# Kernel optimization log

Hardware: AMD Instinct MI355X
Metric: run time of the kernel (lower is better)

## Reference

```python
import jax, jax.numpy as jnp
import numpy as np

S, B, D, H, DH = 512, 32, 256, 8, 32  # seq, batch, in_dim, heads, dim_head
LN_EPS = 1e-5


def setup_inputs() -> dict:
    key = jax.random.key(0)
    k1, k2, k3 = jax.random.split(key, 3)
    x = jax.random.normal(k1, (S, B, D), jnp.float32)
    slow_W = jax.random.normal(k2, (H * (5 * DH + 2), D), jnp.float32) * 0.02
    out_W = jax.random.normal(k3, (D, H * DH), jnp.float32) * 0.02
    ln_g = jnp.ones((D,), jnp.float32)
    ln_b = jnp.zeros((D,), jnp.float32)
    return {"x": x, "slow_W": slow_W, "out_W": out_W, "ln_g": ln_g, "ln_b": ln_b}


def elu_p1(x):
    return jax.nn.elu(x) + 1.0


def sum_norm(x):
    return x / jnp.sum(x, axis=-1, keepdims=True)


def layer_norm(x, g, b):
    mu = jnp.mean(x, axis=-1, keepdims=True)
    var = jnp.mean(jnp.square(x - mu), axis=-1, keepdims=True)
    return (x - mu) * jax.lax.rsqrt(var + LN_EPS) * g + b


def _fast_rnn_forward(x, slow_W, out_W, ln_g, ln_b):
    slen, bsz, _ = x.shape
    o = layer_norm(x, ln_g, ln_b)
    qkv = jnp.einsum('sbd,ed->sbe', o, slow_W)  # [S,B,H*(5*DH+2)]
    qkv = qkv.reshape(slen, bsz, H, 5 * DH + 2)
    q, k, v, rk, rv, beta, rbeta = jnp.split(
        qkv, [DH, 2 * DH, 3 * DH, 4 * DH, 5 * DH, 5 * DH + 1], axis=-1)
    beta = jax.nn.sigmoid(beta)      # [S,B,H,1]
    rbeta = jax.nn.sigmoid(rbeta)    # [S,B,H,1]
    q = sum_norm(elu_p1(q))
    k = sum_norm(elu_p1(k))
    rk = jax.nn.softmax(rk, axis=-1)

    # ---- feed-forward fast weights with delta rule (fast_weight_delta) ----
    def ff_step(W, inp):
        qt, kt, vt, bt = inp                      # [B,H,DH], bt [B,H,1]
        v_old = jnp.einsum('bhij,bhj->bhi', W, kt)
        W = W + ((bt * (vt - v_old))[..., :, None] * kt[..., None, :])
        z = jnp.einsum('bhij,bhj->bhi', W, qt)
        return W, z

    W0 = jnp.zeros((bsz, H, DH, DH), x.dtype)
    _, z = jax.lax.scan(ff_step, W0, (q, k, v, beta))  # z: [S,B,H,DH]

    # ---- recurrent fast weights (fast_rnn_v2): query = softmax(prev state) ----
    def rec_step(carry, inp):
        R, h = carry
        zt, kt, vt, bt = inp
        q_rec = jax.nn.softmax(h, axis=-1)         # query from previous state
        v_old = jnp.einsum('bhij,bhj->bhi', R, kt)
        R = R + ((bt * (vt - v_old))[..., :, None] * kt[..., None, :])
        h = zt + jnp.einsum('bhij,bhj->bhi', R, q_rec)
        return (R, h), h

    R0 = jnp.zeros((bsz, H, DH, DH), x.dtype)
    h0 = jnp.zeros((bsz, H, DH), x.dtype)
    _, hs = jax.lax.scan(rec_step, (R0, h0), (z, rk, rv, rbeta))  # [S,B,H,DH]

    out = hs.reshape(slen, bsz, H * DH)
    out = jnp.einsum('sbe,de->sbd', out, out_W)
    return x + out  # dropout is identity in eval


def reference(x, slow_W, out_W, ln_g, ln_b):
    return _fast_rnn_forward(x, slow_W, out_W, ln_g, ln_b)
```

## Files before the change

### kernel.cpp

```cpp
#include <hip/hip_runtime.h>
#include <hip/hip_bf16.h>
#include <math.h>

#define S_   512
#define B_   32
#define D_   256
#define H_   8
#define DH_  32
#define E_   (H_*(5*DH_+2))
#define SB_  (S_*B_)
#define LN_EPSF 1e-5f

#define ROWP_ 164
#define CH2_  32
#define NC2_  (S_/CH2_)
#define NPAD_ 1344

typedef short  bf16x8 __attribute__((ext_vector_type(8)));
typedef float  f32x4  __attribute__((ext_vector_type(4)));

__device__ __forceinline__ float wave_sum64(float v){
  #pragma unroll
  for (int m = 32; m >= 1; m >>= 1) v += __shfl_xor(v, m, 64);
  return v;
}
__device__ __forceinline__ float gsum32(float v){
  #pragma unroll
  for (int m = 16; m >= 1; m >>= 1) v += __shfl_xor(v, m, 32);
  return v;
}
__device__ __forceinline__ float gmax32(float v){
  #pragma unroll
  for (int m = 16; m >= 1; m >>= 1) v = fmaxf(v, __shfl_xor(v, m, 32));
  return v;
}

#if __has_builtin(__builtin_amdgcn_permlane32_swap)
typedef int v2i_ __attribute__((ext_vector_type(2)));
__device__ __forceinline__ float xhalf_sum(float x){
  v2i_ r = __builtin_amdgcn_permlane32_swap(__float_as_int(x), __float_as_int(x), false, false);
  return __int_as_float(r.x) + __int_as_float(r.y);
}
#else
__device__ __forceinline__ float xhalf_sum(float x){
  return x + __shfl_xor(x, 32, 64);
}
#endif

__device__ __forceinline__ void gl16(const float* g, float* l){
  __builtin_amdgcn_global_load_lds(
      (const __attribute__((address_space(1))) unsigned int*)g,
      (__attribute__((address_space(3))) unsigned int*)l, 16, 0, 0);
}
__device__ __forceinline__ void stage_plane32(const float* gb, int fieldOff,
                                              float* plane, int lane){
  const int tt = lane >> 3, dd = (lane & 7) << 2;
  #pragma unroll
  for (int i = 0; i < 4; i++)
    gl16(gb + (size_t)(8*i + tt)*ROWP_ + fieldOff + dd, plane + i*256);
}
__device__ __forceinline__ void stage_beta32(const float* gb, float* bpl, int lane){
  if (lane < CH2_) gl16(gb + (size_t)lane*ROWP_ + 5*DH_, bpl);
}

__global__ __launch_bounds__(256) void ln_kernel(const float* __restrict__ x,
                                                 const float* __restrict__ g,
                                                 const float* __restrict__ b,
                                                 __hip_bfloat16* __restrict__ o){
  __shared__ float sbuf[4];
  const int row = blockIdx.x, tid = threadIdx.x;
  const float v = x[(size_t)row*D_ + tid];
  float s = wave_sum64(v);
  if ((tid & 63) == 0) sbuf[tid >> 6] = s;
  __syncthreads();
  const float mu = (sbuf[0]+sbuf[1]+sbuf[2]+sbuf[3]) * (1.f/D_);
  __syncthreads();
  const float d = v - mu;
  float s2 = wave_sum64(d*d);
  if ((tid & 63) == 0) sbuf[tid >> 6] = s2;
  __syncthreads();
  const float var = (sbuf[0]+sbuf[1]+sbuf[2]+sbuf[3]) * (1.f/D_);
  const float rstd = rsqrtf(var + LN_EPSF);
  o[(size_t)row*D_ + tid] = __float2bfloat16(d*rstd*g[tid] + b[tid]);
}

__global__ __launch_bounds__(256) void cvt_w1(const float* __restrict__ W,
                                              __hip_bfloat16* __restrict__ o){
  const int r = blockIdx.x, c = threadIdx.x;
  const float v = (r < E_) ? W[(size_t)r*D_ + c] : 0.f;
  o[(size_t)r*D_ + c] = __float2bfloat16(v);
}
__global__ __launch_bounds__(256) void cvt_w2(const float* __restrict__ W,
                                              __hip_bfloat16* __restrict__ o){
  const size_t i = (size_t)blockIdx.x*256 + threadIdx.x;
  o[i] = __float2bfloat16(W[i]);
}

__global__ __launch_bounds__(256) void gemm1_mfma(const __hip_bfloat16* __restrict__ A,
                                                  const __hip_bfloat16* __restrict__ Bw,
                                                  float* __restrict__ qkvT){
  const int tid = threadIdx.x;
  const int w = tid >> 6, l = tid & 63;
  const int lr = l & 15, lk = (l >> 4) << 3;
  const int m0 = blockIdx.y*64 + (w>>1)*32;
  const int n0 = blockIdx.x*64 + (w&1)*32;

  const __hip_bfloat16* Ap = A  + (size_t)(m0+lr)*D_ + lk;
  const __hip_bfloat16* Bp = Bw + (size_t)(n0+lr)*D_ + lk;

  f32x4 acc00={0,0,0,0}, acc01={0,0,0,0}, acc10={0,0,0,0}, acc11={0,0,0,0};
  #pragma unroll
  for (int ks = 0; ks < 8; ++ks){
    const bf16x8 a0 = *(const bf16x8*)(Ap + ks*32);
    const bf16x8 a1 = *(const bf16x8*)(Ap + 16*D_ + ks*32);
    const bf16x8 b0 = *(const bf16x8*)(Bp + ks*32);
    const bf16x8 b1 = *(const bf16x8*)(Bp + 16*D_ + ks*32);
    acc00 = __builtin_amdgcn_mfma_f32_16x16x32_bf16(a0, b0, acc00, 0,0,0);
    acc01 = __builtin_amdgcn_mfma_f32_16x16x32_bf16(a0, b1, acc01, 0,0,0);
    acc10 = __builtin_amdgcn_mfma_f32_16x16x32_bf16(a1, b0, acc10, 0,0,0);
    acc11 = __builtin_amdgcn_mfma_f32_16x16x32_bf16(a1, b1, acc11, 0,0,0);
  }

  const int mrow = (l>>4)<<2;
  #pragma unroll
  for (int i=0;i<2;i++){
    #pragma unroll
    for (int j=0;j<2;j++){
      const f32x4 av = (i==0) ? (j==0?acc00:acc01) : (j==0?acc10:acc11);
      const int n = n0 + j*16 + lr;
      if (n < E_){
        const unsigned head = (unsigned)n / 162u;
        const unsigned jj   = (unsigned)n - head*162u;
        #pragma unroll
        for (int reg=0;reg<4;reg++){
          const int m = m0 + i*16 + mrow + reg;
          const int s = m >> 5, bq = m & 31;
          qkvT[((size_t)(bq*8u+head)*S_ + s)*ROWP_ + jj] = av[reg];
        }
      }
    }
  }
}

__global__ __launch_bounds__(256) void gemm2_mfma(const __hip_bfloat16* __restrict__ A,
                                                  const __hip_bfloat16* __restrict__ Bw,
                                                  const float* __restrict__ X,
                                                  float* __restrict__ C){
  const int tid = threadIdx.x;
  const int w = tid >> 6, l = tid & 63;
  const int lr = l & 15, lk = (l >> 4) << 3;
  const int m0 = blockIdx.y*64 + (w>>1)*32;
  const int n0 = blockIdx.x*64 + (w&1)*32;

  const __hip_bfloat16* Ap = A  + (size_t)(m0+lr)*D_ + lk;
  const __hip_bfloat16* Bp = Bw + (size_t)(n0+lr)*D_ + lk;

  f32x4 acc00={0,0,0,0}, acc01={0,0,0,0}, acc10={0,0,0,0}, acc11={0,0,0,0};
  #pragma unroll
  for (int ks = 0; ks < 8; ++ks){
    const bf16x8 a0 = *(const bf16x8*)(Ap + ks*32);
    const bf16x8 a1 = *(const bf16x8*)(Ap + 16*D_ + ks*32);
    const bf16x8 b0 = *(const bf16x8*)(Bp + ks*32);
    const bf16x8 b1 = *(const bf16x8*)(Bp + 16*D_ + ks*32);
    acc00 = __builtin_amdgcn_mfma_f32_16x16x32_bf16(a0, b0, acc00, 0,0,0);
    acc01 = __builtin_amdgcn_mfma_f32_16x16x32_bf16(a0, b1, acc01, 0,0,0);
    acc10 = __builtin_amdgcn_mfma_f32_16x16x32_bf16(a1, b0, acc10, 0,0,0);
    acc11 = __builtin_amdgcn_mfma_f32_16x16x32_bf16(a1, b1, acc11, 0,0,0);
  }

  const int mrow = (l>>4)<<2;
  #pragma unroll
  for (int i=0;i<2;i++){
    #pragma unroll
    for (int j=0;j<2;j++){
      const f32x4 av = (i==0) ? (j==0?acc00:acc01) : (j==0?acc10:acc11);
      const int n = n0 + j*16 + lr;
      #pragma unroll
      for (int reg=0;reg<4;reg++){
        const size_t m = (size_t)(m0 + i*16 + mrow + reg);
        C[m*D_ + n] = av[reg] + X[m*D_ + n];
      }
    }
  }
}

__global__ __launch_bounds__(256) void act2_kernel(float* __restrict__ qkvT){
  const int row = blockIdx.x*8 + (threadIdx.x >> 5);
  const int i = threadIdx.x & 31;
  float* base = qkvT + (size_t)row*ROWP_;
  float qv  = base[i];
  float kv  = base[DH_ + i];
  float rkv = base[3*DH_ + i];
  qv = qv > 0.f ? qv + 1.f : __expf(qv);
  kv = kv > 0.f ? kv + 1.f : __expf(kv);
  const float qs = gsum32(qv);
  const float ks = gsum32(kv);
  const float rm = gmax32(rkv);
  const float re = __expf(rkv - rm);
  const float rs = gsum32(re);
  base[i]         = qv / qs;
  base[DH_ + i]   = kv / ks;
  base[3*DH_ + i] = re / rs;
  if (i < 2){
    const float bv = base[5*DH_ + i];
    base[5*DH_ + i] = 1.f/(1.f + __expf(-bv));
  }
}

__global__ __launch_bounds__(64,1) void scan_fused(const float* __restrict__ qkvT,
                                                   __hip_bfloat16* __restrict__ hsb){
  const int pair = blockIdx.x;
  const int lane = threadIdx.x;
  const int r = lane & 31, p = lane >> 5;
  const int b = pair >> 3, hh = pair & 7;
  const float* gbase = qkvT + (size_t)pair*S_*ROWP_;

  __shared__ __align__(16) float Lq [2][CH2_][DH_];
  __shared__ __align__(16) float Lk [2][CH2_][DH_];
  __shared__ __align__(16) float Lv [2][CH2_][DH_];
  __shared__ __align__(16) float Lrk[2][CH2_][DH_];
  __shared__ __align__(16) float Lrv[2][CH2_][DH_];
  __shared__ __align__(16) float Lb [2][CH2_][4];
  __shared__ __align__(16) float ebuf[2][DH_];

  float W[16], R[16];
  #pragma unroll
  for (int i=0;i<16;i++){ W[i]=0.f; R[i]=0.f; }
  float h = 0.f;

  stage_plane32(gbase, 0,      &Lq [0][0][0], lane);
  stage_plane32(gbase, DH_,    &Lk [0][0][0], lane);
  stage_plane32(gbase, 2*DH_,  &Lv [0][0][0], lane);
  stage_plane32(gbase, 3*DH_,  &Lrk[0][0][0], lane);
  stage_plane32(gbase, 4*DH_,  &Lrv[0][0][0], lane);
  stage_beta32 (gbase,         &Lb [0][0][0], lane);
  asm volatile("s_waitcnt vmcnt(0)" ::: "memory");

  for (int c = 0; c < NC2_; ++c){
    const int bi = c & 1;
    if (c+1 < NC2_){
      const float* gnext = gbase + (size_t)(c+1)*CH2_*ROWP_;
      stage_plane32(gnext, 0,      &Lq [bi^1][0][0], lane);
      stage_plane32(gnext, DH_,    &Lk [bi^1][0][0], lane);
      stage_plane32(gnext, 2*DH_,  &Lv [bi^1][0][0], lane);
      stage_plane32(gnext, 3*DH_,  &Lrk[bi^1][0][0], lane);
      stage_plane32(gnext, 4*DH_,  &Lrv[bi^1][0][0], lane);
      stage_beta32 (gnext,         &Lb [bi^1][0][0], lane);
    }
    const int s0 = c*CH2_;
    #pragma unroll 2
    for (int t = 0; t < CH2_; ++t){
      const float e = __expf(h);
      if (!p) ebuf[t&1][r] = e;

      float q[16], k[16], rk[16];
      #pragma unroll
      for (int j=0;j<4;j++){
        *(float4*)&q[4*j]  = *(const float4*)&Lq [bi][t][p*16 + 4*j];
        *(float4*)&k[4*j]  = *(const float4*)&Lk [bi][t][p*16 + 4*j];
        *(float4*)&rk[4*j] = *(const float4*)&Lrk[bi][t][p*16 + 4*j];
      }
      const float vv  = Lv [bi][t][r];
      const float rvv = Lrv[bi][t][r];
      const float2 bet = *(const float2*)&Lb[bi][t][0];

      float a0=0.f,a1=0.f,a2=0.f,a3=0.f;
      #pragma unroll
      for (int c4=0;c4<16;c4+=4){
        a0=fmaf(W[c4+0],k[c4+0],a0); a1=fmaf(W[c4+1],k[c4+1],a1);
        a2=fmaf(W[c4+2],k[c4+2],a2); a3=fmaf(W[c4+3],k[c4+3],a3);
      }
      const float dot1f = xhalf_sum((a0+a1)+(a2+a3));
      const float coeff = bet.x*(vv - dot1f);
      float b0=0.f,b1=0.f,b2=0.f,b3=0.f;
      #pragma unroll
      for (int c4=0;c4<16;c4+=4){
        W[c4+0]=fmaf(coeff,k[c4+0],W[c4+0]); b0=fmaf(W[c4+0],q[c4+0],b0);
        W[c4+1]=fmaf(coeff,k[c4+1],W[c4+1]); b1=fmaf(W[c4+1],q[c4+1],b1);
        W[c4+2]=fmaf(coeff,k[c4+2],W[c4+2]); b2=fmaf(W[c4+2],q[c4+2],b2);
        W[c4+3]=fmaf(coeff,k[c4+3],W[c4+3]); b3=fmaf(W[c4+3],q[c4+3],b3);
      }
      const float z = xhalf_sum((b0+b1)+(b2+b3));

      float c0=0.f,c1=0.f,c2=0.f,c3=0.f;
      #pragma unroll
      for (int c4=0;c4<16;c4+=4){
        c0=fmaf(R[c4+0],rk[c4+0],c0); c1=fmaf(R[c4+1],rk[c4+1],c1);
        c2=fmaf(R[c4+2],rk[c4+2],c2); c3=fmaf(R[c4+3],rk[c4+3],c3);
      }
      const float dot1r = xhalf_sum((c0+c1)+(c2+c3));
      const float coefr = bet.y*(rvv - dot1r);
      #pragma unroll
      for (int c4=0;c4<16;c4+=4){
        R[c4+0]=fmaf(coefr,rk[c4+0],R[c4+0]); R[c4+1]=fmaf(coefr,rk[c4+1],R[c4+1]);
        R[c4+2]=fmaf(coefr,rk[c4+2],R[c4+2]); R[c4+3]=fmaf(coefr,rk[c4+3],R[c4+3]);
      }

      float ev[16];
      #pragma unroll
      for (int j=0;j<4;j++)
        *(float4*)&ev[4*j] = *(const float4*)&ebuf[t&1][p*16 + 4*j];

      float t0=(ev[0]+ev[1])+(ev[2]+ev[3]),   t1=(ev[4]+ev[5])+(ev[6]+ev[7]);
      float t2=(ev[8]+ev[9])+(ev[10]+ev[11]), t3=(ev[12]+ev[13])+(ev[14]+ev[15]);
      const float Ss = xhalf_sum((t0+t1)+(t2+t3));

      float d0=0.f,d1=0.f,d2=0.f,d3=0.f;
      #pragma unroll
      for (int c4=0;c4<16;c4+=4){
        d0=fmaf(R[c4+0],ev[c4+0],d0); d1=fmaf(R[c4+1],ev[c4+1],d1);
        d2=fmaf(R[c4+2],ev[c4+2],d2); d3=fmaf(R[c4+3],ev[c4+3],d3);
      }
      const float dot2 = xhalf_sum((d0+d1)+(d2+d3));

      h = fmaf(dot2, __builtin_amdgcn_rcpf(Ss), z);
      if (!p) hsb[((size_t)(s0+t)*B_ + b)*D_ + hh*DH_ + r] = __float2bfloat16(h);
    }
    asm volatile("s_waitcnt vmcnt(0)" ::: "memory");
  }
}

extern "C" void kernel_launch(void* const* d_in, const int* in_sizes, int n_in,
                              void* d_out, int out_size, void* d_ws, size_t ws_size,
                              hipStream_t stream) {
  const float* x      = (const float*)d_in[0];
  const float* slow_W = (const float*)d_in[1];
  const float* out_W  = (const float*)d_in[2];
  const float* ln_g   = (const float*)d_in[3];
  const float* ln_b   = (const float*)d_in[4];
  float* out = (float*)d_out;

  float* qkvT = (float*)d_ws;
  __hip_bfloat16* obf  = (__hip_bfloat16*)(qkvT + (size_t)B_*H_*S_*ROWP_);
  __hip_bfloat16* hsb  = obf;
  __hip_bfloat16* w1bf = obf + (size_t)SB_*D_;
  __hip_bfloat16* w2bf = w1bf + (size_t)NPAD_*D_;

  cvt_w1<<<NPAD_, 256, 0, stream>>>(slow_W, w1bf);
  cvt_w2<<<D_, 256, 0, stream>>>(out_W, w2bf);
  ln_kernel<<<SB_, 256, 0, stream>>>(x, ln_g, ln_b, obf);

  dim3 g1(NPAD_/64, SB_/64);
  gemm1_mfma<<<g1, 256, 0, stream>>>(obf, w1bf, qkvT);

  act2_kernel<<<B_*H_*S_/8, 256, 0, stream>>>(qkvT);

  scan_fused<<<B_*H_, 64, 0, stream>>>(qkvT, hsb);

  dim3 g2(D_/64, SB_/64);
  gemm2_mfma<<<g2, 256, 0, stream>>>(hsb, w2bf, x, out);
}
```

Before: 419.2 us.

## Prefetch scan inputs directly into registers with two-step software pipeline

Replaces the chunked LDS double-buffering in the recurrent scan kernel with direct global-to-register loads via inline asm. Two register sets hold the next two timesteps, and vmcnt waits are set by hand. This removes the LDS staging traffic and the per-chunk full waits. The cost is higher register pressure, a fragile hand-counted vmcnt scheme, and exposed global latency if two steps of lookahead are not enough. The hsb store is now done by all lanes, and the ebuf write is no longer guarded by p.

Measured after the change: 374.5 us. -10.7%, faster.

```diff
diff --git a/kernel.cpp b/kernel.cpp
--- a/kernel.cpp
+++ b/kernel.cpp
@@ -12,12 +12,11 @@
 #define LN_EPSF 1e-5f
 
 #define ROWP_ 164
-#define CH2_  32
-#define NC2_  (S_/CH2_)
 #define NPAD_ 1344
 
 typedef short  bf16x8 __attribute__((ext_vector_type(8)));
 typedef float  f32x4  __attribute__((ext_vector_type(4)));
+typedef float  f32x2  __attribute__((ext_vector_type(2)));
 
 __device__ __forceinline__ float wave_sum64(float v){
   #pragma unroll
@@ -47,21 +46,15 @@
 }
 #endif
 
-__device__ __forceinline__ void gl16(const float* g, float* l){
-  __builtin_amdgcn_global_load_lds(
-      (const __attribute__((address_space(1))) unsigned int*)g,
-      (__attribute__((address_space(3))) unsigned int*)l, 16, 0, 0);
-}
-__device__ __forceinline__ void stage_plane32(const float* gb, int fieldOff,
-                                              float* plane, int lane){
-  const int tt = lane >> 3, dd = (lane & 7) << 2;
-  #pragma unroll
-  for (int i = 0; i < 4; i++)
-    gl16(gb + (size_t)(8*i + tt)*ROWP_ + fieldOff + dd, plane + i*256);
-}
-__device__ __forceinline__ void stage_beta32(const float* gb, float* bpl, int lane){
-  if (lane < CH2_) gl16(gb + (size_t)lane*ROWP_ + 5*DH_, bpl);
-}
+#define GL4(dst, sb, vo, IMM) \
+  asm volatile("global_load_dwordx4 %0, %1, %2 offset:" IMM \
+               : "=&v"(dst) : "v"(vo), "s"(sb))
+#define GL2(dst, sb, vo, IMM) \
+  asm volatile("global_load_dwordx2 %0, %1, %2 offset:" IMM \
+               : "=&v"(dst) : "v"(vo), "s"(sb))
+#define GL1(dst, sb, vo, IMM) \
+  asm volatile("global_load_dword %0, %1, %2 offset:" IMM \
+               : "=&v"(dst) : "v"(vo), "s"(sb))
 
 __global__ __launch_bounds__(256) void ln_kernel(const float* __restrict__ x,
                                                  const float* __restrict__ g,
@@ -207,116 +200,125 @@
   }
 }
 
-__global__ __launch_bounds__(64,1) void scan_fused(const float* __restrict__ qkvT,
-                                                   __hip_bfloat16* __restrict__ hsb){
+#define SCAN_ISSUE(P, sbp)                                                    \
+  { const float* sb_ = (sbp);                                                 \
+    GL4(P##q0,  sb_, voP, "0");   GL4(P##q1,  sb_, voP, "16");                \
+    GL4(P##q2,  sb_, voP, "32");  GL4(P##q3,  sb_, voP, "48");                \
+    GL4(P##k0,  sb_, voP, "128"); GL4(P##k1,  sb_, voP, "144");               \
+    GL4(P##k2,  sb_, voP, "160"); GL4(P##k3,  sb_, voP, "176");               \
+    GL4(P##rk0, sb_, voP, "384"); GL4(P##rk1, sb_, voP, "400");               \
+    GL4(P##rk2, sb_, voP, "416"); GL4(P##rk3, sb_, voP, "432");               \
+    GL1(P##v,   sb_, voR, "256"); GL1(P##rv,  sb_, voR, "512");               \
+    GL2(P##bb,  sb_, voZ, "640"); }
+
+#define SCAN_BODY(P, tt)                                                      \
+  {                                                                           \
+             \
+    const float e_ = __expf(h);                                               \
+    ebuf[r] = e_;                                                             \
+    f32x4 ev0 = *(const f32x4*)&ebuf[p16+0];                                  \
+    f32x4 ev1 = *(const f32x4*)&ebuf[p16+4];                                  \
+    f32x4 ev2 = *(const f32x4*)&ebuf[p16+8];                                  \
+    f32x4 ev3 = *(const f32x4*)&ebuf[p16+12];                                 \
+                                    \
+    if ((tt) >= S_-2) { asm volatile("s_waitcnt vmcnt(0)" ::: "memory"); }    \
+    else              { asm volatile("s_waitcnt vmcnt(16)" ::: "memory"); }   \
+    __builtin_amdgcn_sched_barrier(0);                                        \
+    float q_[16], k_[16], rk_[16];                                            \
+    *(f32x4*)&q_[0]=P##q0;  *(f32x4*)&q_[4]=P##q1;                            \
+    *(f32x4*)&q_[8]=P##q2;  *(f32x4*)&q_[12]=P##q3;                           \
+    *(f32x4*)&k_[0]=P##k0;  *(f32x4*)&k_[4]=P##k1;                            \
+    *(f32x4*)&k_[8]=P##k2;  *(f32x4*)&k_[12]=P##k3;                           \
+    *(f32x4*)&rk_[0]=P##rk0; *(f32x4*)&rk_[4]=P##rk1;                         \
+    *(f32x4*)&rk_[8]=P##rk2; *(f32x4*)&rk_[12]=P##rk3;                        \
+    const float vv = P##v, rvv = P##rv;                                       \
+    const float beta = P##bb.x, rbeta = P##bb.y;                              \
+                                                      \
+    float a0=0.f,a1=0.f,a2=0.f,a3=0.f;                                        \
+    _Pragma("unroll")                                                         \
+    for (int c4=0;c4<16;c4+=4){                                               \
+      a0=fmaf(W[c4+0],k_[c4+0],a0); a1=fmaf(W[c4+1],k_[c4+1],a1);             \
+      a2=fmaf(W[c4+2],k_[c4+2],a2); a3=fmaf(W[c4+3],k_[c4+3],a3);             \
+    }                                                                         \
+    const float dot1f = xhalf_sum((a0+a1)+(a2+a3));                           \
+    const float coeff = beta*(vv - dot1f);                                    \
+    float b0=0.f,b1=0.f,b2=0.f,b3=0.f;                                        \
+    _Pragma("unroll")                                                         \
+    for (int c4=0;c4<16;c4+=4){                                               \
+      W[c4+0]=fmaf(coeff,k_[c4+0],W[c4+0]); b0=fmaf(W[c4+0],q_[c4+0],b0);     \
+      W[c4+1]=fmaf(coeff,k_[c4+1],W[c4+1]); b1=fmaf(W[c4+1],q_[c4+1],b1);     \
+      W[c4+2]=fmaf(coeff,k_[c4+2],W[c4+2]); b2=fmaf(W[c4+2],q_[c4+2],b2);     \
+      W[c4+3]=fmaf(coeff,k_[c4+3],W[c4+3]); b3=fmaf(W[c4+3],q_[c4+3],b3);     \
+    }                                                                         \
+    const float z_ = xhalf_sum((b0+b1)+(b2+b3));                              \
+                            \
+    float c0=0.f,c1=0.f,c2=0.f,c3=0.f;                                        \
+    _Pragma("unroll")                                                         \
+    for (int c4=0;c4<16;c4+=4){                                               \
+      c0=fmaf(R[c4+0],rk_[c4+0],c0); c1=fmaf(R[c4+1],rk_[c4+1],c1);           \
+      c2=fmaf(R[c4+2],rk_[c4+2],c2); c3=fmaf(R[c4+3],rk_[c4+3],c3);           \
+    }                                                                         \
+    const float dot1r = xhalf_sum((c0+c1)+(c2+c3));                           \
+    const float coefr = rbeta*(rvv - dot1r);                                  \
+    _Pragma("unroll")                                                         \
+    for (int c4=0;c4<16;c4+=4){                                               \
+      R[c4+0]=fmaf(coefr,rk_[c4+0],R[c4+0]); R[c4+1]=fmaf(coefr,rk_[c4+1],R[c4+1]); \
+      R[c4+2]=fmaf(coefr,rk_[c4+2],R[c4+2]); R[c4+3]=fmaf(coefr,rk_[c4+3],R[c4+3]); \
+    }                                                                         \
+      \
+    float evv[16];                                                            \
+    *(f32x4*)&evv[0]=ev0; *(f32x4*)&evv[4]=ev1;                               \
+    *(f32x4*)&evv[8]=ev2; *(f32x4*)&evv[12]=ev3;                              \
+    float t0=(evv[0]+evv[1])+(evv[2]+evv[3]),   t1=(evv[4]+evv[5])+(evv[6]+evv[7]); \
+    float t2=(evv[8]+evv[9])+(evv[10]+evv[11]), t3=(evv[12]+evv[13])+(evv[14]+evv[15]); \
+    const float Ss = xhalf_sum((t0+t1)+(t2+t3));                              \
+    float d0=0.f,d1=0.f,d2=0.f,d3=0.f;                                        \
+    _Pragma("unroll")                                                         \
+    for (int c4=0;c4<16;c4+=4){                                               \
+      d0=fmaf(R[c4+0],evv[c4+0],d0); d1=fmaf(R[c4+1],evv[c4+1],d1);           \
+      d2=fmaf(R[c4+2],evv[c4+2],d2); d3=fmaf(R[c4+3],evv[c4+3],d3);           \
+    }                                                                         \
+    const float dot2 = xhalf_sum((d0+d1)+(d2+d3));                            \
+    h = fmaf(dot2, __builtin_amdgcn_rcpf(Ss), z_);                            \
+    hsb[(size_t)(tt)*(B_*D_) + hoff] = __float2bfloat16(h);                   \
+                                       \
+    if ((tt)+2 < S_) SCAN_ISSUE(P, gbase + (size_t)((tt)+2)*ROWP_);           \
+  }
+
+__global__ __launch_bounds__(64,1) void scan_fused2(const float* __restrict__ qkvT,
+                                                    __hip_bfloat16* __restrict__ hsb){
   const int pair = blockIdx.x;
   const int lane = threadIdx.x;
   const int r = lane & 31, p = lane >> 5;
+  const int p16 = p*16;
   const int b = pair >> 3, hh = pair & 7;
   const float* gbase = qkvT + (size_t)pair*S_*ROWP_;
-
-  __shared__ __align__(16) float Lq [2][CH2_][DH_];
-  __shared__ __align__(16) float Lk [2][CH2_][DH_];
-  __shared__ __align__(16) float Lv [2][CH2_][DH_];
-  __shared__ __align__(16) float Lrk[2][CH2_][DH_];
-  __shared__ __align__(16) float Lrv[2][CH2_][DH_];
-  __shared__ __align__(16) float Lb [2][CH2_][4];
-  __shared__ __align__(16) float ebuf[2][DH_];
+  const size_t hoff = (size_t)b*D_ + hh*DH_ + r;
+
+  __shared__ __align__(16) float ebuf[DH_];
+
+  const int voP = p*64;
+  const int voR = r*4;
+  const int voZ = 0;
 
   float W[16], R[16];
   #pragma unroll
   for (int i=0;i<16;i++){ W[i]=0.f; R[i]=0.f; }
   float h = 0.f;
 
-  stage_plane32(gbase, 0,      &Lq [0][0][0], lane);
-  stage_plane32(gbase, DH_,    &Lk [0][0][0], lane);
-  stage_plane32(gbase, 2*DH_,  &Lv [0][0][0], lane);
-  stage_plane32(gbase, 3*DH_,  &Lrk[0][0][0], lane);
-  stage_plane32(gbase, 4*DH_,  &Lrv[0][0][0], lane);
-  stage_beta32 (gbase,         &Lb [0][0][0], lane);
-  asm volatile("s_waitcnt vmcnt(0)" ::: "memory");
-
-  for (int c = 0; c < NC2_; ++c){
-    const int bi = c & 1;
-    if (c+1 < NC2_){
-      const float* gnext = gbase + (size_t)(c+1)*CH2_*ROWP_;
-      stage_plane32(gnext, 0,      &Lq [bi^1][0][0], lane);
-      stage_plane32(gnext, DH_,    &Lk [bi^1][0][0], lane);
-      stage_plane32(gnext, 2*DH_,  &Lv [bi^1][0][0], lane);
-      stage_plane32(gnext, 3*DH_,  &Lrk[bi^1][0][0], lane);
-      stage_plane32(gnext, 4*DH_,  &Lrv[bi^1][0][0], lane);
-      stage_beta32 (gnext,         &Lb [bi^1][0][0], lane);
-    }
-    const int s0 = c*CH2_;
-    #pragma unroll 2
-    for (int t = 0; t < CH2_; ++t){
-      const float e = __expf(h);
-      if (!p) ebuf[t&1][r] = e;
-
-      float q[16], k[16], rk[16];
-      #pragma unroll
-      for (int j=0;j<4;j++){
-        *(float4*)&q[4*j]  = *(const float4*)&Lq [bi][t][p*16 + 4*j];
-        *(float4*)&k[4*j]  = *(const float4*)&Lk [bi][t][p*16 + 4*j];
-        *(float4*)&rk[4*j] = *(const float4*)&Lrk[bi][t][p*16 + 4*j];
-      }
-      const float vv  = Lv [bi][t][r];
-      const float rvv = Lrv[bi][t][r];
-      const float2 bet = *(const float2*)&Lb[bi][t][0];
-
-      float a0=0.f,a1=0.f,a2=0.f,a3=0.f;
-      #pragma unroll
-      for (int c4=0;c4<16;c4+=4){
-        a0=fmaf(W[c4+0],k[c4+0],a0); a1=fmaf(W[c4+1],k[c4+1],a1);
-        a2=fmaf(W[c4+2],k[c4+2],a2); a3=fmaf(W[c4+3],k[c4+3],a3);
-      }
-      const float dot1f = xhalf_sum((a0+a1)+(a2+a3));
-      const float coeff = bet.x*(vv - dot1f);
-      float b0=0.f,b1=0.f,b2=0.f,b3=0.f;
-      #pragma unroll
-      for (int c4=0;c4<16;c4+=4){
-        W[c4+0]=fmaf(coeff,k[c4+0],W[c4+0]); b0=fmaf(W[c4+0],q[c4+0],b0);
-        W[c4+1]=fmaf(coeff,k[c4+1],W[c4+1]); b1=fmaf(W[c4+1],q[c4+1],b1);
-        W[c4+2]=fmaf(coeff,k[c4+2],W[c4+2]); b2=fmaf(W[c4+2],q[c4+2],b2);
-        W[c4+3]=fmaf(coeff,k[c4+3],W[c4+3]); b3=fmaf(W[c4+3],q[c4+3],b3);
-      }
-      const float z = xhalf_sum((b0+b1)+(b2+b3));
-
-      float c0=0.f,c1=0.f,c2=0.f,c3=0.f;
-      #pragma unroll
-      for (int c4=0;c4<16;c4+=4){
-        c0=fmaf(R[c4+0],rk[c4+0],c0); c1=fmaf(R[c4+1],rk[c4+1],c1);
-        c2=fmaf(R[c4+2],rk[c4+2],c2); c3=fmaf(R[c4+3],rk[c4+3],c3);
-      }
-      const float dot1r = xhalf_sum((c0+c1)+(c2+c3));
-      const float coefr = bet.y*(rvv - dot1r);
-      #pragma unroll
-      for (int c4=0;c4<16;c4+=4){
-        R[c4+0]=fmaf(coefr,rk[c4+0],R[c4+0]); R[c4+1]=fmaf(coefr,rk[c4+1],R[c4+1]);
-        R[c4+2]=fmaf(coefr,rk[c4+2],R[c4+2]); R[c4+3]=fmaf(coefr,rk[c4+3],R[c4+3]);
-      }
-
-      float ev[16];
-      #pragma unroll
-      for (int j=0;j<4;j++)
-        *(float4*)&ev[4*j] = *(const float4*)&ebuf[t&1][p*16 + 4*j];
-
-      float t0=(ev[0]+ev[1])+(ev[2]+ev[3]),   t1=(ev[4]+ev[5])+(ev[6]+ev[7]);
-      float t2=(ev[8]+ev[9])+(ev[10]+ev[11]), t3=(ev[12]+ev[13])+(ev[14]+ev[15]);
-      const float Ss = xhalf_sum((t0+t1)+(t2+t3));
-
-      float d0=0.f,d1=0.f,d2=0.f,d3=0.f;
-      #pragma unroll
-      for (int c4=0;c4<16;c4+=4){
-        d0=fmaf(R[c4+0],ev[c4+0],d0); d1=fmaf(R[c4+1],ev[c4+1],d1);
-        d2=fmaf(R[c4+2],ev[c4+2],d2); d3=fmaf(R[c4+3],ev[c4+3],d3);
-      }
-      const float dot2 = xhalf_sum((d0+d1)+(d2+d3));
-
-      h = fmaf(dot2, __builtin_amdgcn_rcpf(Ss), z);
-      if (!p) hsb[((size_t)(s0+t)*B_ + b)*D_ + hh*DH_ + r] = __float2bfloat16(h);
-    }
-    asm volatile("s_waitcnt vmcnt(0)" ::: "memory");
+  f32x4 Aq0,Aq1,Aq2,Aq3, Ak0,Ak1,Ak2,Ak3, Ark0,Ark1,Ark2,Ark3;
+  f32x2 Abb; float Av, Arv;
+  f32x4 Bq0,Bq1,Bq2,Bq3, Bk0,Bk1,Bk2,Bk3, Brk0,Brk1,Brk2,Brk3;
+  f32x2 Bbb; float Bv, Brv;
+
+  SCAN_ISSUE(A, gbase);
+  SCAN_ISSUE(B, gbase + ROWP_);
+  asm volatile("s_waitcnt vmcnt(15)" ::: "memory");
+  __builtin_amdgcn_sched_barrier(0);
+
+  for (int tc = 0; tc < S_; tc += 2){
+    SCAN_BODY(A, tc);
+    SCAN_BODY(B, tc+1);
   }
 }
 
@@ -345,7 +347,7 @@
 
   act2_kernel<<<B_*H_*S_/8, 256, 0, stream>>>(qkvT);
 
-  scan_fused<<<B_*H_, 64, 0, stream>>>(qkvT, hsb);
+  scan_fused2<<<B_*H_, 64, 0, stream>>>(qkvT, hsb);
 
   dim3 g2(D_/64, SB_/64);
   gemm2_mfma<<<g2, 256, 0, stream>>>(hsb, w2bf, x, out);
```
